# Optimization experiments

Measured on AMD Instinct MI355X. Metric: run time of the kernel, lower is better.

Reference implementation:

```python
import jax, jax.numpy as jnp
import numpy as np

N, E, G = 10000, 160000, 64     # nodes, edges, graphs in batch
T, F_IN, F_OUT, L = 5, 75, 15, 4  # towers, per-tower in (divide_input=False), per-tower out, conv layers
AVG_DEG_LOG = float(np.log(17.0))  # stand-in for PyG histogram stat (source deg=zeros -> NaN)
BN_EPS = 1e-5
STD_EPS = 1e-5


def _u(key, shape):
    fi, fo = shape[-2], shape[-1]
    lim = float(np.sqrt(6.0 / (fi + fo)))
    return jax.random.uniform(key, shape, jnp.float32, -lim, lim)


def setup_inputs():
    key = jax.random.key(0)
    k = iter(jax.random.split(key, 24))
    inp = {}
    inp["x"] = jax.random.randint(next(k), (N, 2), 0, 21)
    inp["edge_index"] = jax.random.randint(next(k), (2, E), 0, N)
    inp["edge_attr"] = jax.random.randint(next(k), (E, 2), 0, 4)
    inp["batch"] = jnp.sort(jax.random.randint(next(k), (N,), 0, G))
    inp["node_emb"] = jax.random.normal(next(k), (21, 75), jnp.float32)
    inp["edge_emb"] = jax.random.normal(next(k), (4, 25), jnp.float32)
    inp["pre_lin_W"] = _u(next(k), (150, 75)); inp["pre_lin_b"] = jnp.zeros((75,), jnp.float32)
    inp["edge_enc_W"] = _u(next(k), (L, 50, F_IN)); inp["edge_enc_b"] = jnp.zeros((L, F_IN), jnp.float32)
    inp["pre_W"] = _u(next(k), (L, T, 3 * F_IN, F_IN)); inp["pre_b"] = jnp.zeros((L, T, F_IN), jnp.float32)
    inp["post_W"] = _u(next(k), (L, T, 13 * F_IN, F_OUT)); inp["post_b"] = jnp.zeros((L, T, F_OUT), jnp.float32)
    inp["lin_W"] = _u(next(k), (L, T * F_OUT, 75)); inp["lin_b"] = jnp.zeros((L, 75), jnp.float32)
    inp["bn_g"] = jnp.ones((L, 75), jnp.float32); inp["bn_b"] = jnp.zeros((L, 75), jnp.float32)
    inp["mlp_W1"] = _u(next(k), (75, 50)); inp["mlp_b1"] = jnp.zeros((50,), jnp.float32)
    inp["mlp_W2"] = _u(next(k), (50, 25)); inp["mlp_b2"] = jnp.zeros((25,), jnp.float32)
    inp["mlp_W3"] = _u(next(k), (25, 1)); inp["mlp_b3"] = jnp.zeros((1,), jnp.float32)
    return inp


def _forward(x, edge_index, edge_attr, batch, node_emb, edge_emb, pre_lin_W, pre_lin_b,
             edge_enc_W, edge_enc_b, pre_W, pre_b, post_W, post_b, lin_W, lin_b,
             bn_g, bn_b, mlp_W1, mlp_b1, mlp_W2, mlp_b2, mlp_W3, mlp_b3):
    # node / edge embeddings -> features
    h = node_emb[x].reshape(N, 150) @ pre_lin_W + pre_lin_b          # [N,75]
    ea = edge_emb[edge_attr].reshape(E, 50)                           # [E,50]
    src, dst = edge_index[0], edge_index[1]  # messages flow src -> dst (x_j=src, x_i=dst)

    cnt = jax.ops.segment_sum(jnp.ones((E,), jnp.float32), dst, num_segments=N)  # in-degree [N]
    deg = jnp.maximum(cnt, 1.0)[:, None, None]
    log_deg = jnp.log(jnp.maximum(cnt, 1.0) + 1.0)[:, None, None]
    amp = log_deg / AVG_DEG_LOG
    att = AVG_DEG_LOG / log_deg
    has = (cnt > 0)[:, None, None]

    for l in range(L):
        e = ea @ edge_enc_W[l] + edge_enc_b[l]                        # [E,75]
        m_in = jnp.concatenate([h[dst], h[src], e], axis=-1)          # [E,225]
        msgs = jnp.einsum('ec,tcf->etf', m_in, pre_W[l]) + pre_b[l]   # [E,T,75]
        s = jax.ops.segment_sum(msgs, dst, num_segments=N)
        mean = s / deg
        mean_sq = jax.ops.segment_sum(msgs * msgs, dst, num_segments=N) / deg
        std = jnp.sqrt(jax.nn.relu(mean_sq - mean * mean) + STD_EPS)
        mn = jnp.where(has, jax.ops.segment_min(msgs, dst, num_segments=N), 0.0)
        mx = jnp.where(has, jax.ops.segment_max(msgs, dst, num_segments=N), 0.0)
        agg = jnp.concatenate([mean, mn, mx, std], axis=-1)           # [N,T,300]
        scaled = jnp.concatenate([agg, agg * amp, agg * att], axis=-1)  # [N,T,900]
        out = jnp.concatenate([jnp.broadcast_to(h[:, None, :], (N, T, F_IN)), scaled], axis=-1)  # [N,T,975]
        post = jnp.einsum('ntc,tcf->ntf', out, post_W[l]) + post_b[l]  # [N,T,15]
        hc = post.reshape(N, T * F_OUT) @ lin_W[l] + lin_b[l]          # [N,75]
        mu = hc.mean(axis=0)
        var = hc.var(axis=0)  # biased, matches BatchNorm1d training mode
        h = jax.nn.relu((hc - mu) / jnp.sqrt(var + BN_EPS) * bn_g[l] + bn_b[l])

    g = jax.ops.segment_sum(h, batch, num_segments=G)                 # global_add_pool [G,75]
    g = jax.nn.relu(g @ mlp_W1 + mlp_b1)
    g = jax.nn.relu(g @ mlp_W2 + mlp_b2)
    return g @ mlp_W3 + mlp_b3                                        # [G,1]


def reference(x, edge_index, edge_attr, batch, node_emb, edge_emb, pre_lin_W, pre_lin_b,
              edge_enc_W, edge_enc_b, pre_W, pre_b, post_W, post_b, lin_W, lin_b,
              bn_g, bn_b, mlp_W1, mlp_b1, mlp_W2, mlp_b2, mlp_W3, mlp_b3):
    return _forward(x, edge_index, edge_attr, batch, node_emb, edge_emb, pre_lin_W, pre_lin_b,
                    edge_enc_W, edge_enc_b, pre_W, pre_b, post_W, post_b, lin_W, lin_b,
                    bn_g, bn_b, mlp_W1, mlp_b1, mlp_W2, mlp_b2, mlp_W3, mlp_b3)
```

## Files before the change

kernel.cpp:

```cpp
#include <hip/hip_runtime.h>
#include <hip/hip_bf16.h>
#include <math.h>

#define NN 10000
#define NE 160000
#define NG 64
#define NT 5
#define NL 4
#define ADL 2.833213344056216f

#define OFF_H      0
#define OFF_HC     750000
#define OFF_P      1500000
#define OFF_Q      5250000
#define OFF_AGG    9000000
#define OFF_RLUT   24000000
#define OFF_INVDEG 24006000
#define OFF_AMP    24016000
#define OFF_ATT    24026000
#define OFF_STATS  24036000
#define OFF_GPOOL  24040000
#define OFF_INT    24118960

typedef __attribute__((ext_vector_type(2))) unsigned int uv2;

__device__ __forceinline__ float bf2f(__hip_bfloat16 v){ return __bfloat162float(v); }

__global__ void k_zero_cnt(int* cnt){
    int i = blockIdx.x*256 + threadIdx.x;
    if (i < NN) cnt[i] = 0;
}

__global__ __launch_bounds__(256) void k_h0(const int* __restrict__ x,
        const float* __restrict__ node_emb, const float* __restrict__ plW,
        const float* __restrict__ plb, float* __restrict__ h){
    __shared__ float s_emb[21*75];
    __shared__ float s_W[150*75];
    __shared__ float s_b[75];
    int tid = threadIdx.x;
    for (int i = tid; i < 21*75; i += 256) s_emb[i] = node_emb[i];
    for (int i = tid; i < 150*75; i += 256) s_W[i] = plW[i];
    if (tid < 75) s_b[tid] = plb[tid];
    __syncthreads();
    for (int out = blockIdx.x*256 + tid; out < NN*75; out += gridDim.x*256){
        int n = out / 75, f = out - n*75;
        int x0 = x[2*n], x1 = x[2*n+1];
        float acc = s_b[f];
        const float* e0 = s_emb + x0*75;
        const float* e1 = s_emb + x1*75;
        #pragma unroll 5
        for (int k = 0; k < 75; k++)
            acc += e0[k]*s_W[k*75+f] + e1[k]*s_W[(75+k)*75+f];
        h[out] = acc;
    }
}

__global__ void k_hist(const int* __restrict__ ei, int* __restrict__ cnt){
    int e = blockIdx.x*256 + threadIdx.x;
    if (e < NE) atomicAdd(&cnt[ei[NE + e]], 1);
}

__global__ void k_scan(const int* __restrict__ cnt, int* __restrict__ eoff){
    __shared__ int buf[256];
    __shared__ int carry;
    int tid = threadIdx.x;
    if (tid == 0){ carry = 0; eoff[0] = 0; }
    __syncthreads();
    for (int base = 0; base < NN; base += 256){
        int v = (base + tid < NN) ? cnt[base + tid] : 0;
        buf[tid] = v; __syncthreads();
        for (int off = 1; off < 256; off <<= 1){
            int t2 = (tid >= off) ? buf[tid - off] : 0;
            __syncthreads();
            buf[tid] += t2;
            __syncthreads();
        }
        int inc = buf[tid] + carry;
        if (base + tid < NN) eoff[base + tid + 1] = inc;
        __syncthreads();
        if (tid == 255) carry = inc;
        __syncthreads();
    }
}

__global__ void k_nodestats(const int* __restrict__ cnt, const int* __restrict__ eoff,
        float* __restrict__ invdeg, float* __restrict__ amp, float* __restrict__ att,
        int* __restrict__ cursor){
    int n = blockIdx.x*256 + threadIdx.x;
    if (n >= NN) return;
    int c = cnt[n];
    cursor[n] = eoff[n];
    float cf = (float)c;
    float dg = cf < 1.f ? 1.f : cf;
    invdeg[n] = 1.f / dg;
    float ld = logf(dg + 1.f);
    amp[n] = ld / ADL;
    att[n] = ADL / ld;
}

__global__ void k_scatter(const int* __restrict__ ei, const int* __restrict__ ea,
        int* __restrict__ cursor, int* __restrict__ esrc, int* __restrict__ ecombo){
    int e = blockIdx.x*256 + threadIdx.x;
    if (e >= NE) return;
    int src = ei[e], dst = ei[NE + e];
    int pos = atomicAdd(&cursor[dst], 1);
    esrc[pos] = src;
    ecombo[pos] = ea[2*e]*4 + ea[2*e+1];
}

__global__ __launch_bounds__(384) void k_rlut(
        const float* __restrict__ preW, const float* __restrict__ preb,
        const float* __restrict__ edge_emb, const float* __restrict__ encW,
        const float* __restrict__ encb, int l,
        float* __restrict__ Rlut, float* __restrict__ stats_all){
    __shared__ float smem[10675];
    int tid = threadIdx.x;
    int bx = blockIdx.x;

    if (bx == 5){
        float* stats_wr = stats_all + (l & 1)*192;
        for (int i = tid; i < 150; i += 384) stats_wr[i] = 0.f;
        return;
    }
    int t = bx;
    float* s_encW = smem;
    float* s_ev   = smem + 3750;
    float* s_wc   = smem + 4950;
    float* s_ee   = smem + 10575;
    for (int i = tid; i < 3750; i += 384) s_encW[i] = encW[(size_t)l*3750 + i];
    for (int i = tid; i < 100; i += 384) s_ee[i] = edge_emb[i];
    const float* wcsrc = preW + (((size_t)(l*NT + t))*225 + 150)*75;
    for (int i = tid; i < 5625; i += 384) s_wc[i] = wcsrc[i];
    __syncthreads();
    for (int task = tid; task < 1200; task += 384){
        int b = task/75, m = task - 75*b;
        int a0 = b >> 2, a1 = b & 3;
        float s = encb[l*75 + m];
        for (int k = 0; k < 25; k++)
            s += s_ee[a0*25+k]*s_encW[k*75+m] + s_ee[a1*25+k]*s_encW[(25+k)*75+m];
        s_ev[task] = s;
    }
    __syncthreads();
    for (int task = tid; task < 1200; task += 384){
        int b = task/75, f = task - 75*b;
        float r = preb[((size_t)l*NT + t)*75 + f];
        const float* ev = s_ev + b*75;
        #pragma unroll 5
        for (int m = 0; m < 75; m++) r += ev[m]*s_wc[m*75 + f];
        Rlut[b*375 + t*75 + f] = r;
    }
}

__global__ __launch_bounds__(384) void k_pq(float* __restrict__ h,
        const float* __restrict__ hc, const float* __restrict__ bng,
        const float* __restrict__ bnb,
        const float* __restrict__ preW, const float* __restrict__ preb,
        int l, __hip_bfloat16* __restrict__ P, __hip_bfloat16* __restrict__ Q,
        const float* __restrict__ stats_all){
    __shared__ float h_t[16*76];
    int tid = threadIdx.x;
    int base = blockIdx.x*16;

    if (l == 0){
        for (int idx = tid; idx < 16*75; idx += 384){
            int i = idx/75, m = idx - 75*i;
            int n = base + i;
            h_t[i*76 + m] = (n < NN) ? h[(size_t)n*75 + m] : 0.f;
        }
    } else {
        const float* stats_rd = stats_all + ((l + 1) & 1)*192;
        int lp = l - 1;
        for (int idx = tid; idx < 16*75; idx += 384){
            int i = idx/75, m = idx - 75*i;
            int n = base + i;
            float v = 0.f;
            if (n < NN){
                float mu = stats_rd[m]*(1.0f/NN);
                float var = stats_rd[75+m]*(1.0f/NN) - mu*mu;
                float inv = rsqrtf(var + 1e-5f);
                v = (hc[(size_t)n*75 + m] - mu)*inv*bng[lp*75+m] + bnb[lp*75+m];
                v = v > 0.f ? v : 0.f;
                h[(size_t)n*75 + m] = v;
            }
            h_t[i*76 + m] = v;
        }
    }
    __syncthreads();
    int j = tid;
    if (j >= 375) return;
    int t = j/75, f = j - 75*t;
    const float* wbase = preW + ((size_t)(l*NT + t))*225*75 + f;
    float accP[16], accQ[16];
    #pragma unroll
    for (int i = 0; i < 16; i++){ accP[i] = 0.f; accQ[i] = 0.f; }
    for (int m = 0; m < 72; m += 4){
        float wa0 = wbase[(m+0)*75], wa1 = wbase[(m+1)*75];
        float wa2 = wbase[(m+2)*75], wa3 = wbase[(m+3)*75];
        float wb0 = wbase[(75+m+0)*75], wb1 = wbase[(75+m+1)*75];
        float wb2 = wbase[(75+m+2)*75], wb3 = wbase[(75+m+3)*75];
        #pragma unroll
        for (int i = 0; i < 16; i++){
            const float4 hv = *(const float4*)&h_t[i*76 + m];
            accP[i] += hv.x*wa0 + hv.y*wa1 + hv.z*wa2 + hv.w*wa3;
            accQ[i] += hv.x*wb0 + hv.y*wb1 + hv.z*wb2 + hv.w*wb3;
        }
    }
    for (int m = 72; m < 75; m++){
        float wa = wbase[m*75], wb = wbase[(75+m)*75];
        #pragma unroll
        for (int i = 0; i < 16; i++){
            float v = h_t[i*76 + m];
            accP[i] += v*wa; accQ[i] += v*wb;
        }
    }
    for (int i = 0; i < 16; i++){
        int n = base + i;
        if (n < NN){
            P[(size_t)n*375 + j] = __float2bfloat16(accP[i]);
            Q[(size_t)n*375 + j] = __float2bfloat16(accQ[i]);
        }
    }
}

__global__ __launch_bounds__(64) void k_agg(const __hip_bfloat16* __restrict__ P,
        const __hip_bfloat16* __restrict__ Q, const float* __restrict__ Rlut,
        const int* __restrict__ eoff, const int* __restrict__ esrc,
        const int* __restrict__ ecombo, const float* __restrict__ invdeg,
        __hip_bfloat16* __restrict__ agg){
    int n = blockIdx.y;
    int j = blockIdx.x*64 + threadIdx.x;
    if (j >= 375) return;
    int lo = eoff[n], hi = eoff[n+1];
    float p = bf2f(P[(size_t)n*375 + j]);
    float sum = 0.f, sq = 0.f, mn = 3.4e38f, mx = -3.4e38f;
    int e = lo;
    for (; e + 8 <= hi; e += 8){
        int s0 = esrc[e],   s1 = esrc[e+1], s2 = esrc[e+2], s3 = esrc[e+3];
        int s4 = esrc[e+4], s5 = esrc[e+5], s6 = esrc[e+6], s7 = esrc[e+7];
        int c0 = ecombo[e],   c1 = ecombo[e+1], c2 = ecombo[e+2], c3 = ecombo[e+3];
        int c4 = ecombo[e+4], c5 = ecombo[e+5], c6 = ecombo[e+6], c7 = ecombo[e+7];
        float q0 = bf2f(Q[(size_t)s0*375 + j]);
        float q1 = bf2f(Q[(size_t)s1*375 + j]);
        float q2 = bf2f(Q[(size_t)s2*375 + j]);
        float q3 = bf2f(Q[(size_t)s3*375 + j]);
        float q4 = bf2f(Q[(size_t)s4*375 + j]);
        float q5 = bf2f(Q[(size_t)s5*375 + j]);
        float q6 = bf2f(Q[(size_t)s6*375 + j]);
        float q7 = bf2f(Q[(size_t)s7*375 + j]);
        float r0 = Rlut[c0*375 + j], r1 = Rlut[c1*375 + j];
        float r2 = Rlut[c2*375 + j], r3 = Rlut[c3*375 + j];
        float r4 = Rlut[c4*375 + j], r5 = Rlut[c5*375 + j];
        float r6 = Rlut[c6*375 + j], r7 = Rlut[c7*375 + j];
        float m0 = p + q0 + r0, m1 = p + q1 + r1;
        float m2 = p + q2 + r2, m3 = p + q3 + r3;
        float m4 = p + q4 + r4, m5 = p + q5 + r5;
        float m6 = p + q6 + r6, m7 = p + q7 + r7;
        sum += (m0 + m1 + m2 + m3) + (m4 + m5 + m6 + m7);
        sq  += (m0*m0 + m1*m1 + m2*m2 + m3*m3) + (m4*m4 + m5*m5 + m6*m6 + m7*m7);
        mn = fminf(mn, fminf(fminf(fminf(m0,m1), fminf(m2,m3)),
                             fminf(fminf(m4,m5), fminf(m6,m7))));
        mx = fmaxf(mx, fmaxf(fmaxf(fmaxf(m0,m1), fmaxf(m2,m3)),
                             fmaxf(fmaxf(m4,m5), fmaxf(m6,m7))));
    }
    for (; e < hi; e++){
        int s = esrc[e], cm = ecombo[e];
        float m = p + bf2f(Q[(size_t)s*375 + j]) + Rlut[cm*375 + j];
        sum += m; sq += m*m;
        mn = fminf(mn, m); mx = fmaxf(mx, m);
    }
    float id = invdeg[n];
    bool has = hi > lo;
    float mean = sum*id;
    float msq  = sq*id;
    float var = msq - mean*mean; var = var > 0.f ? var : 0.f;
    float sd = sqrtf(var + 1e-5f);
    float mnv = has ? mn : 0.f;
    float mxv = has ? mx : 0.f;
    int t = j/75, f = j - 75*t;
    __hip_bfloat16* a = agg + ((size_t)n*NT + t)*300;
    a[f]      = __float2bfloat16(mean);
    a[75+f]   = __float2bfloat16(mnv);
    a[150+f]  = __float2bfloat16(mxv);
    a[225+f]  = __float2bfloat16(sd);
}

#define KB2 50
__global__ __launch_bounds__(256, 4) void k_post(const float* __restrict__ h,
        const __hip_bfloat16* __restrict__ agg, const float* __restrict__ postW,
        const float* __restrict__ postb, const float* __restrict__ amp,
        const float* __restrict__ att, int l, __hip_bfloat16* __restrict__ postbase){
    __shared__ float s_w[3*KB2*16];
    __shared__ unsigned short s_a[256*52];
    int t = blockIdx.y;
    int z = blockIdx.z;
    int nbase = blockIdx.x*256;
    int tid = threadIdx.x;
    int fg  = (tid & 3)*4;
    int sub = tid >> 2;
    const float* Wt = postW + ((size_t)(l*NT + t))*975*15;

    if (z == 0){
        for (int idx = tid; idx < 75*16; idx += 256){
            int c = idx >> 4, f = idx & 15;
            s_w[idx] = (f < 15) ? Wt[c*15 + f] : 0.f;
        }
        __syncthreads();
        float a1[4][4] = {};
        const float* hrow[4];
        #pragma unroll
        for (int j = 0; j < 4; j++){
            int n = nbase + sub + 64*j;
            hrow[j] = h + (size_t)(n < NN ? n : 0)*75;
        }
        #pragma unroll 3
        for (int k = 0; k < 75; k++){
            const float4 w1 = *(const float4*)&s_w[k*16 + fg];
            #pragma unroll
            for (int j = 0; j < 4; j++){
                float v = hrow[j][k];
                a1[j][0] += v*w1.x; a1[j][1] += v*w1.y;
                a1[j][2] += v*w1.z; a1[j][3] += v*w1.w;
            }
        }
        const float* pb = postb + (l*NT + t)*15;
        #pragma unroll
        for (int j = 0; j < 4; j++){
            int n = nbase + sub + 64*j;
            if (n >= NN) continue;
            __hip_bfloat16* dst = postbase + (size_t)n*75 + t*15;
            #pragma unroll
            for (int f = 0; f < 4; f++)
                if (fg + f < 15) dst[fg + f] = __float2bfloat16(a1[j][f] + pb[fg + f]);
        }
        return;
    }

    int kbeg = (z-1)*KB2;
    for (int idx = tid; idx < 3*KB2*16; idx += 256){
        int vrow = idx / (KB2*16);
        int rem = idx - vrow*(KB2*16);
        int c = rem >> 4, f = rem & 15;
        s_w[idx] = (f < 15) ? Wt[(75 + vrow*300 + kbeg + c)*15 + f] : 0.f;
    }
    {
        const unsigned short* asrc = (const unsigned short*)agg;
        for (int idx = tid; idx < 256*25; idx += 256){
            int i = idx/25, w = idx - 25*i;
            int n = nbase + i;
            unsigned int u = 0;
            if (n < NN)
                u = *(const unsigned int*)(asrc + (size_t)n*1500 + t*300 + kbeg + 2*w);
            *(unsigned int*)&s_a[i*52 + 2*w] = u;
        }
    }
    __syncthreads();

    float a1[4][4] = {}, a2[4][4] = {}, a3[4][4] = {};
    const unsigned short* ap0 = s_a + sub*52;
    #pragma unroll 2
    for (int k4 = 0; k4 < 48; k4 += 4){
        uv2 ua[4];
        #pragma unroll
        for (int j = 0; j < 4; j++)
            ua[j] = *(const uv2*)(ap0 + j*(64*52) + k4);
        #pragma unroll
        for (int kk = 0; kk < 4; kk++){
            int k = k4 + kk;
            const float4 w1 = *(const float4*)&s_w[k*16 + fg];
            const float4 w2 = *(const float4*)&s_w[(KB2 + k)*16 + fg];
            const float4 w3 = *(const float4*)&s_w[(2*KB2 + k)*16 + fg];
            #pragma unroll
            for (int j = 0; j < 4; j++){
                unsigned int bits = (kk < 2) ? ua[j].x : ua[j].y;
                float v = __uint_as_float((kk & 1) ? (bits & 0xffff0000u)
                                                   : (bits << 16));
                a1[j][0] += v*w1.x; a1[j][1] += v*w1.y;
                a1[j][2] += v*w1.z; a1[j][3] += v*w1.w;
                a2[j][0] += v*w2.x; a2[j][1] += v*w2.y;
                a2[j][2] += v*w2.z; a2[j][3] += v*w2.w;
                a3[j][0] += v*w3.x; a3[j][1] += v*w3.y;
                a3[j][2] += v*w3.z; a3[j][3] += v*w3.w;
            }
        }
    }
    {
        unsigned int ut[4];
        #pragma unroll
        for (int j = 0; j < 4; j++)
            ut[j] = *(const unsigned int*)(ap0 + j*(64*52) + 48);
        #pragma unroll
        for (int kk = 0; kk < 2; kk++){
            int k = 48 + kk;
            const float4 w1 = *(const float4*)&s_w[k*16 + fg];
            const float4 w2 = *(const float4*)&s_w[(KB2 + k)*16 + fg];
            const float4 w3 = *(const float4*)&s_w[(2*KB2 + k)*16 + fg];
            #pragma unroll
            for (int j = 0; j < 4; j++){
                float v = __uint_as_float((kk & 1) ? (ut[j] & 0xffff0000u)
                                                   : (ut[j] << 16));
                a1[j][0] += v*w1.x; a1[j][1] += v*w1.y;
                a1[j][2] += v*w1.z; a1[j][3] += v*w1.w;
                a2[j][0] += v*w2.x; a2[j][1] += v*w2.y;
                a2[j][2] += v*w2.z; a2[j][3] += v*w2.w;
                a3[j][0] += v*w3.x; a3[j][1] += v*w3.y;
                a3[j][2] += v*w3.z; a3[j][3] += v*w3.w;
            }
        }
    }
    __hip_bfloat16* postv = postbase + (size_t)z*750000;
    #pragma unroll
    for (int j = 0; j < 4; j++){
        int n = nbase + sub + 64*j;
        if (n >= NN) continue;
        float am = amp[n], at = att[n];
        __hip_bfloat16* dst = postv + (size_t)n*75 + t*15;
        #pragma unroll
        for (int f = 0; f < 4; f++)
            if (fg + f < 15)
                dst[fg + f] = __float2bfloat16(a1[j][f] + am*a2[j][f] + at*a3[j][f]);
    }
}

__global__ __launch_bounds__(256) void k_lin(const __hip_bfloat16* __restrict__ postbase,
        const float* __restrict__ linW, const float* __restrict__ linb,
        int l, float* __restrict__ hc, float* __restrict__ stats_all){
    __shared__ float p_l[32*75];
    __shared__ float w_l[75*75];
    __shared__ float hc_l[32*75];
    int tid = threadIdx.x;
    int base = blockIdx.x*32;
    for (int i = tid; i < 75*75; i += 256) w_l[i] = linW[(size_t)l*5625 + i];
    for (int i = tid; i < 32*75; i += 256){
        int n = base + i/75;
        size_t idx = (size_t)base*75 + i;
        float v = 0.f;
        if (n < NN){
            #pragma unroll
            for (int z = 0; z < 7; z++) v += bf2f(postbase[idx + (size_t)z*750000]);
        }
        p_l[i] = v;
    }
    __syncthreads();
    for (int task = tid; task < 2400; task += 256){
        int i = task/75, o = task - 75*i;
        float s = linb[l*75 + o];
        const float* pl = p_l + i*75;
        #pragma unroll 5
        for (int j = 0; j < 75; j++) s += pl[j]*w_l[j*75 + o];
        hc_l[task] = s;
        if (base + i < NN) hc[(size_t)(base+i)*75 + o] = s;
    }
    __syncthreads();
    if (tid < 75){
        float* stats_wr = stats_all + (l & 1)*192;
        int nv = NN - base; if (nv > 32) nv = 32;
        float s1 = 0.f, s2 = 0.f;
        for (int i = 0; i < nv; i++){
            float v = hc_l[i*75 + tid];
            s1 += v; s2 += v*v;
        }
        atomicAdd(&stats_wr[tid], s1);
        atomicAdd(&stats_wr[75+tid], s2);
    }
}

__global__ void k_bnapply(const float* __restrict__ hc, const float* __restrict__ stats,
        const float* __restrict__ bng, const float* __restrict__ bnb, int l,
        float* __restrict__ h){
    int idx = blockIdx.x*256 + threadIdx.x;
    if (idx >= NN*75) return;
    int col = idx % 75;
    float mu = stats[col]*(1.0f/NN);
    float var = stats[75+col]*(1.0f/NN) - mu*mu;
    float inv = rsqrtf(var + 1e-5f);
    float v = (hc[idx] - mu)*inv*bng[l*75+col] + bnb[l*75+col];
    h[idx] = v > 0.f ? v : 0.f;
}

__global__ __launch_bounds__(256) void k_pool(const float* __restrict__ h,
        const int* __restrict__ batch, float* __restrict__ gpool){
    int g = blockIdx.x, tid = threadIdx.x;
    int lo = 0, hi = NN;
    while (lo < hi){ int mid = (lo+hi)>>1; if (batch[mid] < g) lo = mid+1; else hi = mid; }
    int start = lo;
    lo = start; hi = NN;
    while (lo < hi){ int mid = (lo+hi)>>1; if (batch[mid] < g+1) lo = mid+1; else hi = mid; }
    int end = lo;
    __shared__ float red[225];
    if (tid < 225){
        int col = tid % 75, rep = tid / 75;
        float acc = 0.f;
        for (int i = start + rep; i < end; i += 3) acc += h[(size_t)i*75 + col];
        red[tid] = acc;
    }
    __syncthreads();
    if (tid < 75) gpool[g*75 + tid] = red[tid] + red[75+tid] + red[150+tid];
}

__global__ __launch_bounds__(256) void k_mlp(const float* __restrict__ gpool,
        const float* __restrict__ W1, const float* __restrict__ b1,
        const float* __restrict__ W2, const float* __restrict__ b2,
        const float* __restrict__ W3, const float* __restrict__ b3,
        float* __restrict__ out){
    __shared__ float w1[75*50];
    __shared__ float w2[50*25];
    __shared__ float gp[8*75];
    __shared__ float t1[8*50];
    __shared__ float t2[8*25];
    int tid = threadIdx.x;
    int gbase = blockIdx.x*8;
    for (int i = tid; i < 75*50; i += 256) w1[i] = W1[i];
    for (int i = tid; i < 50*25; i += 256) w2[i] = W2[i];
    for (int i = tid; i < 8*75; i += 256) gp[i] = gpool[gbase*75 + i];
    __syncthreads();
    for (int task = tid; task < 8*50; task += 256){
        int g = task/50, j = task - 50*g;
        float s = b1[j];
        const float* gv = gp + g*75;
        #pragma unroll 5
        for (int k = 0; k < 75; k++) s += gv[k]*w1[k*50+j];
        t1[task] = s > 0.f ? s : 0.f;
    }
    __syncthreads();
    for (int task = tid; task < 8*25; task += 256){
        int g = task/25, j = task - 25*g;
        float s = b2[j];
        const float* tv = t1 + g*50;
        #pragma unroll 5
        for (int k = 0; k < 50; k++) s += tv[k]*w2[k*25+j];
        t2[task] = s > 0.f ? s : 0.f;
    }
    __syncthreads();
    if (tid < 8){
        float s = b3[0];
        const float* tv = t2 + tid*25;
        #pragma unroll
        for (int k = 0; k < 25; k++) s += tv[k]*W3[k];
        out[gbase + tid] = s;
    }
}

extern "C" void kernel_launch(void* const* d_in, const int* in_sizes, int n_in,
                              void* d_out, int out_size, void* d_ws, size_t ws_size,
                              hipStream_t stream){
    const int* x          = (const int*)d_in[0];
    const int* edge_index = (const int*)d_in[1];
    const int* edge_attr  = (const int*)d_in[2];
    const int* batch      = (const int*)d_in[3];
    const float* node_emb = (const float*)d_in[4];
    const float* edge_emb = (const float*)d_in[5];
    const float* pre_lin_W= (const float*)d_in[6];
    const float* pre_lin_b= (const float*)d_in[7];
    const float* encW     = (const float*)d_in[8];
    const float* encb     = (const float*)d_in[9];
    const float* preW     = (const float*)d_in[10];
    const float* preb     = (const float*)d_in[11];
    const float* postW    = (const float*)d_in[12];
    const float* postb    = (const float*)d_in[13];
    const float* linW     = (const float*)d_in[14];
    const float* linb     = (const float*)d_in[15];
    const float* bng      = (const float*)d_in[16];
    const float* bnb      = (const float*)d_in[17];
    const float* mlpW1    = (const float*)d_in[18];
    const float* mlpb1    = (const float*)d_in[19];
    const float* mlpW2    = (const float*)d_in[20];
    const float* mlpb2    = (const float*)d_in[21];
    const float* mlpW3    = (const float*)d_in[22];
    const float* mlpb3    = (const float*)d_in[23];

    float* ws = (float*)d_ws;
    float* h      = ws + OFF_H;
    float* hc     = ws + OFF_HC;
    __hip_bfloat16* P = (__hip_bfloat16*)(ws + OFF_P);
    __hip_bfloat16* Q = (__hip_bfloat16*)(ws + OFF_Q);
    __hip_bfloat16* agg = (__hip_bfloat16*)(ws + OFF_AGG);
    float* Rlut   = ws + OFF_RLUT;
    float* invdeg = ws + OFF_INVDEG;
    float* amp    = ws + OFF_AMP;
    float* att    = ws + OFF_ATT;
    float* stats  = ws + OFF_STATS;
    float* gpool  = ws + OFF_GPOOL;
    __hip_bfloat16* postbase = (__hip_bfloat16*)(ws + OFF_P);
    int* iw     = (int*)(ws + OFF_INT);
    int* cnt    = iw;
    int* eoff   = cnt + NN;
    int* cursor = eoff + NN + 2;
    int* esrc   = cursor + NN;
    int* ecombo = esrc + NE;

    k_zero_cnt<<<40, 256, 0, stream>>>(cnt);
    k_h0<<<640, 256, 0, stream>>>(x, node_emb, pre_lin_W, pre_lin_b, h);
    k_hist<<<625, 256, 0, stream>>>(edge_index, cnt);
    k_scan<<<1, 256, 0, stream>>>(cnt, eoff);
    k_nodestats<<<40, 256, 0, stream>>>(cnt, eoff, invdeg, amp, att, cursor);
    k_scatter<<<625, 256, 0, stream>>>(edge_index, edge_attr, cursor, esrc, ecombo);

    for (int l = 0; l < NL; l++){
        k_rlut<<<6, 384, 0, stream>>>(preW, preb, edge_emb, encW, encb, l, Rlut, stats);
        k_pq<<<626, 384, 0, stream>>>(h, hc, bng, bnb, preW, preb, l, P, Q, stats);
        k_agg<<<dim3(6, NN), 64, 0, stream>>>(P, Q, Rlut, eoff, esrc, ecombo, invdeg, agg);
        k_post<<<dim3(40, 5, 7), 256, 0, stream>>>(h, agg, postW, postb, amp, att, l, postbase);
        k_lin<<<313, 256, 0, stream>>>(postbase, linW, linb, l, hc, stats);
    }

    k_bnapply<<<2930, 256, 0, stream>>>(hc, stats + ((NL-1)&1)*192, bng, bnb, NL-1, h);
    k_pool<<<NG, 256, 0, stream>>>(h, batch, gpool);
    k_mlp<<<8, 256, 0, stream>>>(gpool, mlpW1, mlpb1, mlpW2, mlpb2, mlpW3, mlpb3, (float*)d_out);
}
```

Measured before the change: 914.2 us.

## Hoist edge LUTs out of layer loop, transpose pre weights, shrink node tiles

Computes all four layers' edge lookup tables in one launch before the layer loop. The stats zeroing moves into an extra block of k_pq. Pre-transformation weights are transposed once into padded rows, so k_pq loads contiguous float4 weights instead of strided scalars. k_pq and k_post now process half as many nodes per block with higher occupancy targets, giving more blocks and fewer registers per thread at the cost of less weight reuse per block.

```diff
diff --git a/kernel.cpp b/kernel.cpp
--- a/kernel.cpp
+++ b/kernel.cpp
@@ -14,7 +14,8 @@
 #define OFF_P      1500000
 #define OFF_Q      5250000
 #define OFF_AGG    9000000
-#define OFF_RLUT   24000000
+#define OFF_RLUT4  16500000
+#define OFF_PWT    16530000
 #define OFF_INVDEG 24006000
 #define OFF_AMP    24016000
 #define OFF_ATT    24026000
@@ -108,21 +109,27 @@
     ecombo[pos] = ea[2*e]*4 + ea[2*e+1];
 }
 
-__global__ __launch_bounds__(384) void k_rlut(
+__global__ __launch_bounds__(256) void k_wt(const float* __restrict__ preW,
+        float* __restrict__ preW_T){
+    int idx = blockIdx.x*256 + threadIdx.x;
+    if (idx >= 20*75*152) return;
+    int row = idx / 152;
+    int m = idx - row*152;
+    int lt = row / 75, f = row - lt*75;
+    float v = 0.f;
+    if (m < 75)                  v = preW[((size_t)lt*225 + m)*75 + f];
+    else if (m >= 76 && m < 151) v = preW[((size_t)lt*225 + (m - 76) + 75)*75 + f];
+    preW_T[idx] = v;
+}
+
+__global__ __launch_bounds__(384) void k_rlut4(
         const float* __restrict__ preW, const float* __restrict__ preb,
         const float* __restrict__ edge_emb, const float* __restrict__ encW,
-        const float* __restrict__ encb, int l,
-        float* __restrict__ Rlut, float* __restrict__ stats_all){
+        const float* __restrict__ encb, float* __restrict__ rlut_all){
     __shared__ float smem[10675];
     int tid = threadIdx.x;
-    int bx = blockIdx.x;
-
-    if (bx == 5){
-        float* stats_wr = stats_all + (l & 1)*192;
-        for (int i = tid; i < 150; i += 384) stats_wr[i] = 0.f;
-        return;
-    }
-    int t = bx;
+    int t = blockIdx.x;
+    int l = blockIdx.y;
     float* s_encW = smem;
     float* s_ev   = smem + 3750;
     float* s_wc   = smem + 4950;
@@ -147,34 +154,41 @@
         const float* ev = s_ev + b*75;
         #pragma unroll 5
         for (int m = 0; m < 75; m++) r += ev[m]*s_wc[m*75 + f];
-        Rlut[b*375 + t*75 + f] = r;
+        rlut_all[(size_t)l*6000 + b*375 + t*75 + f] = r;
     }
 }
 
 __global__ __launch_bounds__(384) void k_pq(float* __restrict__ h,
         const float* __restrict__ hc, const float* __restrict__ bng,
         const float* __restrict__ bnb,
-        const float* __restrict__ preW, const float* __restrict__ preb,
+        const float* __restrict__ preW_T,
         int l, __hip_bfloat16* __restrict__ P, __hip_bfloat16* __restrict__ Q,
-        const float* __restrict__ stats_all){
-    __shared__ float h_t[16*76];
+        float* __restrict__ stats_all){
+    __shared__ float h_t[8*76];
     int tid = threadIdx.x;
-    int base = blockIdx.x*16;
+    int bx = blockIdx.x;
+
+    if (bx == 1250){
+        float* stats_wr = stats_all + (l & 1)*192;
+        for (int i = tid; i < 150; i += 384) stats_wr[i] = 0.f;
+        return;
+    }
+    int base = bx*8;
 
     if (l == 0){
-        for (int idx = tid; idx < 16*75; idx += 384){
-            int i = idx/75, m = idx - 75*i;
+        for (int idx = tid; idx < 8*76; idx += 384){
+            int i = idx/76, m = idx - 76*i;
             int n = base + i;
-            h_t[i*76 + m] = (n < NN) ? h[(size_t)n*75 + m] : 0.f;
+            h_t[idx] = (m < 75 && n < NN) ? h[(size_t)n*75 + m] : 0.f;
         }
     } else {
         const float* stats_rd = stats_all + ((l + 1) & 1)*192;
         int lp = l - 1;
-        for (int idx = tid; idx < 16*75; idx += 384){
-            int i = idx/75, m = idx - 75*i;
+        for (int idx = tid; idx < 8*76; idx += 384){
+            int i = idx/76, m = idx - 76*i;
             int n = base + i;
             float v = 0.f;
-            if (n < NN){
+            if (m < 75 && n < NN){
                 float mu = stats_rd[m]*(1.0f/NN);
                 float var = stats_rd[75+m]*(1.0f/NN) - mu*mu;
                 float inv = rsqrtf(var + 1e-5f);
@@ -182,38 +196,28 @@
                 v = v > 0.f ? v : 0.f;
                 h[(size_t)n*75 + m] = v;
             }
-            h_t[i*76 + m] = v;
+            h_t[idx] = v;
         }
     }
     __syncthreads();
     int j = tid;
     if (j >= 375) return;
-    int t = j/75, f = j - 75*t;
-    const float* wbase = preW + ((size_t)(l*NT + t))*225*75 + f;
-    float accP[16], accQ[16];
+    const float* wrow = preW_T + ((size_t)(l*NT)*75 + j)*152;
+    float accP[8], accQ[8];
     #pragma unroll
-    for (int i = 0; i < 16; i++){ accP[i] = 0.f; accQ[i] = 0.f; }
-    for (int m = 0; m < 72; m += 4){
-        float wa0 = wbase[(m+0)*75], wa1 = wbase[(m+1)*75];
-        float wa2 = wbase[(m+2)*75], wa3 = wbase[(m+3)*75];
-        float wb0 = wbase[(75+m+0)*75], wb1 = wbase[(75+m+1)*75];
-        float wb2 = wbase[(75+m+2)*75], wb3 = wbase[(75+m+3)*75];
-        #pragma unroll
-        for (int i = 0; i < 16; i++){
+    for (int i = 0; i < 8; i++){ accP[i] = 0.f; accQ[i] = 0.f; }
+    for (int m = 0; m < 76; m += 4){
+        const float4 wa = *(const float4*)&wrow[m];
+        const float4 wb = *(const float4*)&wrow[76 + m];
+        #pragma unroll
+        for (int i = 0; i < 8; i++){
             const float4 hv = *(const float4*)&h_t[i*76 + m];
-            accP[i] += hv.x*wa0 + hv.y*wa1 + hv.z*wa2 + hv.w*wa3;
-            accQ[i] += hv.x*wb0 + hv.y*wb1 + hv.z*wb2 + hv.w*wb3;
-        }
-    }
-    for (int m = 72; m < 75; m++){
-        float wa = wbase[m*75], wb = wbase[(75+m)*75];
-        #pragma unroll
-        for (int i = 0; i < 16; i++){
-            float v = h_t[i*76 + m];
-            accP[i] += v*wa; accQ[i] += v*wb;
-        }
-    }
-    for (int i = 0; i < 16; i++){
+            accP[i] += hv.x*wa.x + hv.y*wa.y + hv.z*wa.z + hv.w*wa.w;
+            accQ[i] += hv.x*wb.x + hv.y*wb.y + hv.z*wb.z + hv.w*wb.w;
+        }
+    }
+    #pragma unroll
+    for (int i = 0; i < 8; i++){
         int n = base + i;
         if (n < NN){
             P[(size_t)n*375 + j] = __float2bfloat16(accP[i]);
@@ -285,15 +289,15 @@
 }
 
 #define KB2 50
-__global__ __launch_bounds__(256, 4) void k_post(const float* __restrict__ h,
+__global__ __launch_bounds__(256, 6) void k_post(const float* __restrict__ h,
         const __hip_bfloat16* __restrict__ agg, const float* __restrict__ postW,
         const float* __restrict__ postb, const float* __restrict__ amp,
         const float* __restrict__ att, int l, __hip_bfloat16* __restrict__ postbase){
     __shared__ float s_w[3*KB2*16];
-    __shared__ unsigned short s_a[256*52];
+    __shared__ unsigned short s_a[128*52];
     int t = blockIdx.y;
     int z = blockIdx.z;
-    int nbase = blockIdx.x*256;
+    int nbase = blockIdx.x*128;
     int tid = threadIdx.x;
     int fg  = (tid & 3)*4;
     int sub = tid >> 2;
@@ -305,10 +309,10 @@
             s_w[idx] = (f < 15) ? Wt[c*15 + f] : 0.f;
         }
         __syncthreads();
-        float a1[4][4] = {};
-        const float* hrow[4];
-        #pragma unroll
-        for (int j = 0; j < 4; j++){
+        float a1[2][4] = {};
+        const float* hrow[2];
+        #pragma unroll
+        for (int j = 0; j < 2; j++){
             int n = nbase + sub + 64*j;
             hrow[j] = h + (size_t)(n < NN ? n : 0)*75;
         }
@@ -316,7 +320,7 @@
         for (int k = 0; k < 75; k++){
             const float4 w1 = *(const float4*)&s_w[k*16 + fg];
             #pragma unroll
-            for (int j = 0; j < 4; j++){
+            for (int j = 0; j < 2; j++){
                 float v = hrow[j][k];
                 a1[j][0] += v*w1.x; a1[j][1] += v*w1.y;
                 a1[j][2] += v*w1.z; a1[j][3] += v*w1.w;
@@ -324,7 +328,7 @@
         }
         const float* pb = postb + (l*NT + t)*15;
         #pragma unroll
-        for (int j = 0; j < 4; j++){
+        for (int j = 0; j < 2; j++){
             int n = nbase + sub + 64*j;
             if (n >= NN) continue;
             __hip_bfloat16* dst = postbase + (size_t)n*75 + t*15;
@@ -344,7 +348,7 @@
     }
     {
         const unsigned short* asrc = (const unsigned short*)agg;
-        for (int idx = tid; idx < 256*25; idx += 256){
+        for (int idx = tid; idx < 128*25; idx += 256){
             int i = idx/25, w = idx - 25*i;
             int n = nbase + i;
             unsigned int u = 0;
@@ -355,13 +359,13 @@
     }
     __syncthreads();
 
-    float a1[4][4] = {}, a2[4][4] = {}, a3[4][4] = {};
+    float a1[2][4] = {}, a2[2][4] = {}, a3[2][4] = {};
     const unsigned short* ap0 = s_a + sub*52;
     #pragma unroll 2
     for (int k4 = 0; k4 < 48; k4 += 4){
-        uv2 ua[4];
-        #pragma unroll
-        for (int j = 0; j < 4; j++)
+        uv2 ua[2];
+        #pragma unroll
+        for (int j = 0; j < 2; j++)
             ua[j] = *(const uv2*)(ap0 + j*(64*52) + k4);
         #pragma unroll
         for (int kk = 0; kk < 4; kk++){
@@ -370,7 +374,7 @@
             const float4 w2 = *(const float4*)&s_w[(KB2 + k)*16 + fg];
             const float4 w3 = *(const float4*)&s_w[(2*KB2 + k)*16 + fg];
             #pragma unroll
-            for (int j = 0; j < 4; j++){
+            for (int j = 0; j < 2; j++){
                 unsigned int bits = (kk < 2) ? ua[j].x : ua[j].y;
                 float v = __uint_as_float((kk & 1) ? (bits & 0xffff0000u)
                                                    : (bits << 16));
@@ -384,9 +388,9 @@
         }
     }
     {
-        unsigned int ut[4];
-        #pragma unroll
-        for (int j = 0; j < 4; j++)
+        unsigned int ut[2];
+        #pragma unroll
+        for (int j = 0; j < 2; j++)
             ut[j] = *(const unsigned int*)(ap0 + j*(64*52) + 48);
         #pragma unroll
         for (int kk = 0; kk < 2; kk++){
@@ -395,7 +399,7 @@
             const float4 w2 = *(const float4*)&s_w[(KB2 + k)*16 + fg];
             const float4 w3 = *(const float4*)&s_w[(2*KB2 + k)*16 + fg];
             #pragma unroll
-            for (int j = 0; j < 4; j++){
+            for (int j = 0; j < 2; j++){
                 float v = __uint_as_float((kk & 1) ? (ut[j] & 0xffff0000u)
                                                    : (ut[j] << 16));
                 a1[j][0] += v*w1.x; a1[j][1] += v*w1.y;
@@ -409,7 +413,7 @@
     }
     __hip_bfloat16* postv = postbase + (size_t)z*750000;
     #pragma unroll
-    for (int j = 0; j < 4; j++){
+    for (int j = 0; j < 2; j++){
         int n = nbase + sub + 64*j;
         if (n >= NN) continue;
         float am = amp[n], at = att[n];
@@ -574,7 +578,8 @@
     __hip_bfloat16* P = (__hip_bfloat16*)(ws + OFF_P);
     __hip_bfloat16* Q = (__hip_bfloat16*)(ws + OFF_Q);
     __hip_bfloat16* agg = (__hip_bfloat16*)(ws + OFF_AGG);
-    float* Rlut   = ws + OFF_RLUT;
+    float* rlut4  = ws + OFF_RLUT4;
+    float* preW_T = ws + OFF_PWT;
     float* invdeg = ws + OFF_INVDEG;
     float* amp    = ws + OFF_AMP;
     float* att    = ws + OFF_ATT;
@@ -589,6 +594,8 @@
     int* ecombo = esrc + NE;
 
     k_zero_cnt<<<40, 256, 0, stream>>>(cnt);
+    k_wt<<<891, 256, 0, stream>>>(preW, preW_T);
+    k_rlut4<<<dim3(5, 4), 384, 0, stream>>>(preW, preb, edge_emb, encW, encb, rlut4);
     k_h0<<<640, 256, 0, stream>>>(x, node_emb, pre_lin_W, pre_lin_b, h);
     k_hist<<<625, 256, 0, stream>>>(edge_index, cnt);
     k_scan<<<1, 256, 0, stream>>>(cnt, eoff);
@@ -596,10 +603,10 @@
     k_scatter<<<625, 256, 0, stream>>>(edge_index, edge_attr, cursor, esrc, ecombo);
 
     for (int l = 0; l < NL; l++){
-        k_rlut<<<6, 384, 0, stream>>>(preW, preb, edge_emb, encW, encb, l, Rlut, stats);
-        k_pq<<<626, 384, 0, stream>>>(h, hc, bng, bnb, preW, preb, l, P, Q, stats);
-        k_agg<<<dim3(6, NN), 64, 0, stream>>>(P, Q, Rlut, eoff, esrc, ecombo, invdeg, agg);
-        k_post<<<dim3(40, 5, 7), 256, 0, stream>>>(h, agg, postW, postb, amp, att, l, postbase);
+        k_pq<<<1251, 384, 0, stream>>>(h, hc, bng, bnb, preW_T, l, P, Q, stats);
+        k_agg<<<dim3(6, NN), 64, 0, stream>>>(P, Q, rlut4 + (size_t)l*6000,
+                                              eoff, esrc, ecombo, invdeg, agg);
+        k_post<<<dim3(79, 5, 7), 256, 0, stream>>>(h, agg, postW, postb, amp, att, l, postbase);
         k_lin<<<313, 256, 0, stream>>>(postbase, linW, linb, l, hc, stats);
     }
 
```

Result: slower. 957.8 us (+4.8%).
